# Optimization experiments

Measured on AMD Instinct MI355X. Metric: run time of the kernel, lower is better.

The kernel has to match this reference:

```python
import jax, jax.numpy as jnp
import numpy as np

B, C, N = 2, 128, 784  # batch, channels, spatial tokens (28x28)
TEMPERATURE = 11.313708498984761  # sqrt(C)


def setup_inputs() -> dict:
    key = jax.random.key(0)
    kq, kk, kv = jax.random.split(key, 3)
    q = jax.random.normal(kq, (B, C, N), dtype=jnp.float32)
    k = jax.random.normal(kk, (B, C, N), dtype=jnp.float32)
    v = jax.random.normal(kv, (B, C, N), dtype=jnp.float32)
    return {"q": q, "k": k, "v": v}


def reference(q, k, v):
    # dist_func == 'l1' branch of ScaledDotProductAttention (eval mode, dropout=0)
    qs = q / TEMPERATURE                                   # [B, C, Nq]
    # torch: q.unsqueeze(2).repeat -> [B,C,Nk,Nq]; k.unsqueeze(3).repeat -> [B,C,Nk,Nq]
    # broadcast instead of repeat; mean over channel dim 1
    diff = jnp.abs(qs[:, :, None, :] - k[:, :, :, None])   # [B, C, Nk, Nq]
    attn = jnp.mean(diff, axis=1)                          # [B, Nk, Nq]
    attn = jax.nn.softmax(attn, axis=-1)                   # softmax over Nq (last dim)
    # torch.bmm(v, attn.permute(0,2,1)): out[b,c,k] = sum_q v[b,c,q] * attn[b,k,q]
    out = jnp.einsum("bcq,bkq->bck", v, attn)              # [B, C, Nk]
    return (out, attn)
```

## Files before the change

kernel.cpp:

```cpp
#include <hip/hip_runtime.h>
#include <math.h>

constexpr int kB = 2;
constexpr int kC = 128;
constexpr int kN = 784;
constexpr float kInvT = 1.0f / 11.313708498984761f;
constexpr float kInvC = 1.0f / 128.0f;

constexpr size_t kOutElems  = (size_t)kB * kC * kN;
constexpr size_t kAttnElems = (size_t)kB * kN * kN;

__device__ inline float wave_max(float v) {
#pragma unroll
    for (int o = 32; o > 0; o >>= 1) v = fmaxf(v, __shfl_xor(v, o, 64));
    return v;
}
__device__ inline float wave_sum(float v) {
#pragma unroll
    for (int o = 32; o > 0; o >>= 1) v += __shfl_xor(v, o, 64);
    return v;
}

constexpr int TK = 64;
constexpr int TQ = 64;
constexpr int NKT = (kN + TK - 1) / TK;
constexpr int NQT = (kN + TQ - 1) / TQ;
constexpr int CSP = 2;
constexpr int CH = kC / CSP;
constexpr int DSTR = 68;

template <bool USE_WS>
__global__ __launch_bounds__(256) void dist_kernel(const float* __restrict__ qg,
                                                   const float* __restrict__ kg,
                                                   float* __restrict__ D0,
                                                   float* __restrict__ D1) {
    int bid = blockIdx.x;
    const int qt = bid % NQT; bid /= NQT;
    const int kt = bid % NKT; bid /= NKT;
    const int ch = bid & 1;   bid >>= 1;
    const int b  = bid;
    const int k0 = kt * TK;
    const int q0 = qt * TQ;
    const int t  = threadIdx.x;

    __shared__ float ks[CH][DSTR];
    __shared__ float qs[CH][DSTR];

    const float* kb = kg + ((size_t)b * kC + ch * CH) * kN;
    const float* qb = qg + ((size_t)b * kC + ch * CH) * kN;

#pragma unroll
    for (int i = t; i < CH * 16; i += 256) {
        const int c  = i >> 4;
        const int x4 = (i & 15) << 2;
        *reinterpret_cast<float4*>(&ks[c][x4]) =
            *reinterpret_cast<const float4*>(kb + (size_t)c * kN + min(k0 + x4, kN - 4));
        float4 qv = *reinterpret_cast<const float4*>(qb + (size_t)c * kN + min(q0 + x4, kN - 4));
        qv.x *= kInvT; qv.y *= kInvT; qv.z *= kInvT; qv.w *= kInvT;
        *reinterpret_cast<float4*>(&qs[c][x4]) = qv;
    }
    __syncthreads();

    const int qx = (t & 15) << 2;
    const int kx = (t >> 4) << 2;

    float acc[4][4];
#pragma unroll
    for (int i = 0; i < 4; ++i)
#pragma unroll
        for (int j = 0; j < 4; ++j) acc[i][j] = 0.0f;

#pragma unroll 4
    for (int c = 0; c < CH; ++c) {
        const float4 kv = *reinterpret_cast<const float4*>(&ks[c][kx]);
        const float4 qv = *reinterpret_cast<const float4*>(&qs[c][qx]);
        const float kf[4] = {kv.x, kv.y, kv.z, kv.w};
        const float qf[4] = {qv.x, qv.y, qv.z, qv.w};
#pragma unroll
        for (int i = 0; i < 4; ++i)
#pragma unroll
            for (int j = 0; j < 4; ++j)
                acc[i][j] += fabsf(qf[j] - kf[i]);
    }

    const int qcol = q0 + qx;
    if (qcol < kN) {
        float* dst = (USE_WS && ch) ? D1 : D0;
#pragma unroll
        for (int i = 0; i < 4; ++i) {
            const int krow = k0 + kx + i;
            if (krow < kN) {
                const size_t off = ((size_t)b * kN + krow) * kN + qcol;
                if (USE_WS) {
                    *reinterpret_cast<float4*>(dst + off) =
                        make_float4(acc[i][0], acc[i][1], acc[i][2], acc[i][3]);
                } else {
                    atomicAdd(&D0[off + 0], acc[i][0]);
                    atomicAdd(&D0[off + 1], acc[i][1]);
                    atomicAdd(&D0[off + 2], acc[i][2]);
                    atomicAdd(&D0[off + 3], acc[i][3]);
                }
            }
        }
    }
}

template <bool SUM2>
__global__ __launch_bounds__(256) void softmax_kernel(float* __restrict__ A,
                                                      const float* __restrict__ W) {
    const size_t row = (size_t)blockIdx.x * kN;
    float4* A4 = reinterpret_cast<float4*>(A + row);
    const float4* W4 = reinterpret_cast<const float4*>(W + row);
    const int t = threadIdx.x;
    const int lane = t & 63, wid = t >> 6;
    const bool act = t < (kN / 4);
    __shared__ float xred[4];

    float4 x = make_float4(-1e30f, -1e30f, -1e30f, -1e30f);
    if (act) {
        x = A4[t];
        if (SUM2) {
            const float4 w = W4[t];
            x.x += w.x; x.y += w.y; x.z += w.z; x.w += w.w;
        }
    }

    float m = fmaxf(fmaxf(x.x, x.y), fmaxf(x.z, x.w));
    m = wave_max(m);
    if (lane == 0) xred[wid] = m;
    __syncthreads();
    m = fmaxf(fmaxf(xred[0], xred[1]), fmaxf(xred[2], xred[3]));
    __syncthreads();

    float4 p;
    p.x = __expf((x.x - m) * kInvC);
    p.y = __expf((x.y - m) * kInvC);
    p.z = __expf((x.z - m) * kInvC);
    p.w = __expf((x.w - m) * kInvC);
    float lsum = p.x + p.y + p.z + p.w;
    lsum = wave_sum(lsum);
    if (lane == 0) xred[wid] = lsum;
    __syncthreads();
    const float inv = 1.0f / (xred[0] + xred[1] + xred[2] + xred[3]);
    if (act) {
        p.x *= inv; p.y *= inv; p.z *= inv; p.w *= inv;
        A4[t] = p;
    }
}

constexpr int BKT = 64;
constexpr int NKT2 = (kN + BKT - 1) / BKT;
constexpr int QSP = 14;
constexpr int QPB = kN / QSP;
constexpr int QCH = 28;
constexpr int BSTR = 68;

template <bool ATOMIC>
__global__ __launch_bounds__(256) void bmm_stage1(const float* __restrict__ vg,
                                                  const float* __restrict__ attn,
                                                  float* __restrict__ P) {
    int bid = blockIdx.x;
    const int qs = bid % QSP;   bid /= QSP;
    const int kt = bid % NKT2;  bid /= NKT2;
    const int ct = bid & 1;     bid >>= 1;
    const int b  = bid;
    const int k0 = kt * BKT;
    const int c0 = ct * 64;
    const int qb0 = qs * QPB;
    const int t  = threadIdx.x;

    __shared__ float vT[QCH][BSTR];
    __shared__ float aT[QCH][BSTR];

    const int cc = t >> 2;
    const int j1 = t & 3;
    const int j2 = j1 + 4;
    const int c0l = (t >> 4) << 2;
    const int k0l = (t & 15) << 2;

    float acc[4][4];
#pragma unroll
    for (int i = 0; i < 4; ++i)
#pragma unroll
        for (int j = 0; j < 4; ++j) acc[i][j] = 0.0f;

    const float* vb = vg + ((size_t)b * kC + c0) * kN;
    const float* ab = attn + (size_t)b * kN * kN;
    const int krow_st = min(k0 + cc, kN - 1);

    for (int qc = 0; qc < QPB; qc += QCH) {
        const int q0 = qb0 + qc;
        const float4 vv1 = *reinterpret_cast<const float4*>(vb + (size_t)cc * kN + q0 + 4 * j1);
        const float4 av1 = *reinterpret_cast<const float4*>(ab + (size_t)krow_st * kN + q0 + 4 * j1);
        float4 vv2, av2;
        const bool has2 = (j2 < 7);
        if (has2) {
            vv2 = *reinterpret_cast<const float4*>(vb + (size_t)cc * kN + q0 + 4 * j2);
            av2 = *reinterpret_cast<const float4*>(ab + (size_t)krow_st * kN + q0 + 4 * j2);
        }
        __syncthreads();
        {
            const int r1 = 4 * j1;
            vT[r1 + 0][cc] = vv1.x; vT[r1 + 1][cc] = vv1.y;
            vT[r1 + 2][cc] = vv1.z; vT[r1 + 3][cc] = vv1.w;
            aT[r1 + 0][cc] = av1.x; aT[r1 + 1][cc] = av1.y;
            aT[r1 + 2][cc] = av1.z; aT[r1 + 3][cc] = av1.w;
            if (has2) {
                const int r2 = 4 * j2;
                vT[r2 + 0][cc] = vv2.x; vT[r2 + 1][cc] = vv2.y;
                vT[r2 + 2][cc] = vv2.z; vT[r2 + 3][cc] = vv2.w;
                aT[r2 + 0][cc] = av2.x; aT[r2 + 1][cc] = av2.y;
                aT[r2 + 2][cc] = av2.z; aT[r2 + 3][cc] = av2.w;
            }
        }
        __syncthreads();

#pragma unroll
        for (int qq = 0; qq < QCH; ++qq) {
            const float4 vf4 = *reinterpret_cast<const float4*>(&vT[qq][c0l]);
            const float4 af4 = *reinterpret_cast<const float4*>(&aT[qq][k0l]);
            const float vf[4] = {vf4.x, vf4.y, vf4.z, vf4.w};
            const float af[4] = {af4.x, af4.y, af4.z, af4.w};
#pragma unroll
            for (int i = 0; i < 4; ++i)
#pragma unroll
                for (int j = 0; j < 4; ++j) acc[i][j] += vf[i] * af[j];
        }
    }

    if (ATOMIC) {
#pragma unroll
        for (int i = 0; i < 4; ++i) {
            const int c = c0 + c0l + i;
#pragma unroll
            for (int j = 0; j < 4; ++j) {
                const int krow = k0 + k0l + j;
                if (krow < kN)
                    atomicAdd(&P[((size_t)b * kC + c) * kN + krow], acc[i][j]);
            }
        }
    } else if (k0 + k0l < kN) {
#pragma unroll
        for (int i = 0; i < 4; ++i) {
            const int c = c0 + c0l + i;
            *reinterpret_cast<float4*>(
                P + (((size_t)qs * kB + b) * kC + c) * kN + k0 + k0l) =
                make_float4(acc[i][0], acc[i][1], acc[i][2], acc[i][3]);
        }
    }
}

__global__ __launch_bounds__(256) void reduce_kernel(const float* __restrict__ P,
                                                     float* __restrict__ out) {
    const int idx = blockIdx.x * 256 + threadIdx.x;
    const float4* p = reinterpret_cast<const float4*>(P) + idx;
    float4 s = p[0];
#pragma unroll
    for (int qs = 1; qs < QSP; ++qs) {
        const float4 v = p[(size_t)qs * (kOutElems / 4)];
        s.x += v.x; s.y += v.y; s.z += v.z; s.w += v.w;
    }
    reinterpret_cast<float4*>(out)[idx] = s;
}

extern "C" void kernel_launch(void* const* d_in, const int* in_sizes, int n_in,
                              void* d_out, int out_size, void* d_ws, size_t ws_size,
                              hipStream_t stream) {
    const float* q = (const float*)d_in[0];
    const float* k = (const float*)d_in[1];
    const float* v = (const float*)d_in[2];

    float* out  = (float*)d_out;
    float* attn = out + kOutElems;
    float* P    = (float*)d_ws;
    float* D1   = P + (size_t)QSP * kOutElems;

    const size_t need = ((size_t)QSP * kOutElems + kAttnElems) * sizeof(float);

    if (ws_size >= need) {
        dist_kernel<true><<<kB * CSP * NKT * NQT, 256, 0, stream>>>(q, k, attn, D1);
        softmax_kernel<true><<<kB * kN, 256, 0, stream>>>(attn, D1);
        bmm_stage1<false><<<kB * 2 * NKT2 * QSP, 256, 0, stream>>>(v, attn, P);
        reduce_kernel<<<(int)(kOutElems / 4 / 256), 256, 0, stream>>>(P, out);
    } else {
        hipMemsetAsync(attn, 0, kAttnElems * sizeof(float), stream);
        hipMemsetAsync(out, 0, kOutElems * sizeof(float), stream);
        dist_kernel<false><<<kB * CSP * NKT * NQT, 256, 0, stream>>>(q, k, attn, nullptr);
        softmax_kernel<false><<<kB * kN, 256, 0, stream>>>(attn, attn);
        bmm_stage1<true><<<kB * 2 * NKT2 * QSP, 256, 0, stream>>>(v, attn, out);
    }
}
```

Before: 93.44 us.

## Replace split-K FP32 bmm and reduce with single fp16 MFMA GEMM kernel

The final v·attnᵀ product now runs in one kernel using 16x16x32 fp16 MFMA instructions. It stages v and attn tiles in shared memory as fp16, with register prefetch of the next K chunk. The previous version split the Q dimension 14 ways, wrote partial results to a workspace and summed them in a separate reduce kernel. That pass and its workspace traffic are gone, but the grid drops to 52 blocks, which underfills the GPU, and the inputs lose precision when converted to fp16.

```diff
diff --git a/kernel.cpp b/kernel.cpp
--- a/kernel.cpp
+++ b/kernel.cpp
@@ -148,119 +148,107 @@
     }
 }
 
-constexpr int BKT = 64;
-constexpr int NKT2 = (kN + BKT - 1) / BKT;
-constexpr int QSP = 14;
-constexpr int QPB = kN / QSP;
-constexpr int QCH = 28;
-constexpr int BSTR = 68;
-
-template <bool ATOMIC>
-__global__ __launch_bounds__(256) void bmm_stage1(const float* __restrict__ vg,
-                                                  const float* __restrict__ attn,
-                                                  float* __restrict__ P) {
+typedef _Float16 half4v __attribute__((ext_vector_type(4)));
+typedef _Float16 half8v __attribute__((ext_vector_type(8)));
+typedef float f32x4 __attribute__((ext_vector_type(4)));
+
+constexpr int GM = 64;
+constexpr int GN = 64;
+constexpr int GK = 128;
+constexpr int NCH = (kN + GK - 1) / GK;
+constexpr int NKT3 = (kN + GN - 1) / GN;
+constexpr int LSTR = 136;
+
+__global__ __launch_bounds__(256) void bmm_mfma(const float* __restrict__ vg,
+                                                const float* __restrict__ attn,
+                                                float* __restrict__ out) {
     int bid = blockIdx.x;
-    const int qs = bid % QSP;   bid /= QSP;
-    const int kt = bid % NKT2;  bid /= NKT2;
-    const int ct = bid & 1;     bid >>= 1;
+    const int kt = bid % NKT3; bid /= NKT3;
+    const int ct = bid & 1;    bid >>= 1;
     const int b  = bid;
-    const int k0 = kt * BKT;
-    const int c0 = ct * 64;
-    const int qb0 = qs * QPB;
+    const int k0 = kt * GN;
+    const int c0 = ct * GM;
     const int t  = threadIdx.x;
-
-    __shared__ float vT[QCH][BSTR];
-    __shared__ float aT[QCH][BSTR];
-
-    const int cc = t >> 2;
-    const int j1 = t & 3;
-    const int j2 = j1 + 4;
-    const int c0l = (t >> 4) << 2;
-    const int k0l = (t & 15) << 2;
-
-    float acc[4][4];
-#pragma unroll
-    for (int i = 0; i < 4; ++i)
-#pragma unroll
-        for (int j = 0; j < 4; ++j) acc[i][j] = 0.0f;
+    const int lane = t & 63;
+    const int w = t >> 6;
+
+    __shared__ _Float16 vs[GM][LSTR];
+    __shared__ _Float16 as_[GN][LSTR];
 
     const float* vb = vg + ((size_t)b * kC + c0) * kN;
     const float* ab = attn + (size_t)b * kN * kN;
-    const int krow_st = min(k0 + cc, kN - 1);
-
-    for (int qc = 0; qc < QPB; qc += QCH) {
-        const int q0 = qb0 + qc;
-        const float4 vv1 = *reinterpret_cast<const float4*>(vb + (size_t)cc * kN + q0 + 4 * j1);
-        const float4 av1 = *reinterpret_cast<const float4*>(ab + (size_t)krow_st * kN + q0 + 4 * j1);
-        float4 vv2, av2;
-        const bool has2 = (j2 < 7);
-        if (has2) {
-            vv2 = *reinterpret_cast<const float4*>(vb + (size_t)cc * kN + q0 + 4 * j2);
-            av2 = *reinterpret_cast<const float4*>(ab + (size_t)krow_st * kN + q0 + 4 * j2);
-        }
+
+    const int col4 = t & 31;
+    const int rb   = t >> 5;
+
+    float4 pv[8], pa[8];
+
+    auto load_chunk = [&](int chnk) {
+        const int qv = chnk * GK + 4 * col4;
+        const bool qok = qv < kN;
+#pragma unroll
+        for (int i = 0; i < 8; ++i) {
+            const int row = rb + 8 * i;
+            pv[i] = qok ? *reinterpret_cast<const float4*>(vb + (size_t)row * kN + qv)
+                        : make_float4(0.f, 0.f, 0.f, 0.f);
+            const int krow = k0 + row;
+            pa[i] = (qok && krow < kN)
+                        ? *reinterpret_cast<const float4*>(ab + (size_t)krow * kN + qv)
+                        : make_float4(0.f, 0.f, 0.f, 0.f);
+        }
+    };
+
+    auto store_chunk = [&]() {
+        const int col = 4 * col4;
+#pragma unroll
+        for (int i = 0; i < 8; ++i) {
+            const int row = rb + 8 * i;
+            half4v hv = {(_Float16)pv[i].x, (_Float16)pv[i].y,
+                         (_Float16)pv[i].z, (_Float16)pv[i].w};
+            *reinterpret_cast<half4v*>(&vs[row][col]) = hv;
+            half4v ha = {(_Float16)pa[i].x, (_Float16)pa[i].y,
+                         (_Float16)pa[i].z, (_Float16)pa[i].w};
+            *reinterpret_cast<half4v*>(&as_[row][col]) = ha;
+        }
+    };
+
+    f32x4 acc[4] = {};
+
+    const int arow = 16 * w + (lane & 15);
+    const int brow0 = lane & 15;
+    const int kgrp = (lane >> 4) * 8;
+
+    load_chunk(0);
+    for (int chnk = 0; chnk < NCH; ++chnk) {
         __syncthreads();
-        {
-            const int r1 = 4 * j1;
-            vT[r1 + 0][cc] = vv1.x; vT[r1 + 1][cc] = vv1.y;
-            vT[r1 + 2][cc] = vv1.z; vT[r1 + 3][cc] = vv1.w;
-            aT[r1 + 0][cc] = av1.x; aT[r1 + 1][cc] = av1.y;
-            aT[r1 + 2][cc] = av1.z; aT[r1 + 3][cc] = av1.w;
-            if (has2) {
-                const int r2 = 4 * j2;
-                vT[r2 + 0][cc] = vv2.x; vT[r2 + 1][cc] = vv2.y;
-                vT[r2 + 2][cc] = vv2.z; vT[r2 + 3][cc] = vv2.w;
-                aT[r2 + 0][cc] = av2.x; aT[r2 + 1][cc] = av2.y;
-                aT[r2 + 2][cc] = av2.z; aT[r2 + 3][cc] = av2.w;
+        store_chunk();
+        __syncthreads();
+        if (chnk + 1 < NCH) load_chunk(chnk + 1);
+
+#pragma unroll
+        for (int ks = 0; ks < GK / 32; ++ks) {
+            const int koff = ks * 32 + kgrp;
+            const half8v av = *reinterpret_cast<const half8v*>(&vs[arow][koff]);
+#pragma unroll
+            for (int n = 0; n < 4; ++n) {
+                const half8v bv =
+                    *reinterpret_cast<const half8v*>(&as_[16 * n + brow0][koff]);
+                acc[n] = __builtin_amdgcn_mfma_f32_16x16x32_f16(av, bv, acc[n], 0, 0, 0);
             }
         }
-        __syncthreads();
-
-#pragma unroll
-        for (int qq = 0; qq < QCH; ++qq) {
-            const float4 vf4 = *reinterpret_cast<const float4*>(&vT[qq][c0l]);
-            const float4 af4 = *reinterpret_cast<const float4*>(&aT[qq][k0l]);
-            const float vf[4] = {vf4.x, vf4.y, vf4.z, vf4.w};
-            const float af[4] = {af4.x, af4.y, af4.z, af4.w};
-#pragma unroll
-            for (int i = 0; i < 4; ++i)
-#pragma unroll
-                for (int j = 0; j < 4; ++j) acc[i][j] += vf[i] * af[j];
-        }
-    }
-
-    if (ATOMIC) {
-#pragma unroll
-        for (int i = 0; i < 4; ++i) {
-            const int c = c0 + c0l + i;
-#pragma unroll
-            for (int j = 0; j < 4; ++j) {
-                const int krow = k0 + k0l + j;
-                if (krow < kN)
-                    atomicAdd(&P[((size_t)b * kC + c) * kN + krow], acc[i][j]);
-            }
-        }
-    } else if (k0 + k0l < kN) {
-#pragma unroll
-        for (int i = 0; i < 4; ++i) {
-            const int c = c0 + c0l + i;
-            *reinterpret_cast<float4*>(
-                P + (((size_t)qs * kB + b) * kC + c) * kN + k0 + k0l) =
-                make_float4(acc[i][0], acc[i][1], acc[i][2], acc[i][3]);
-        }
-    }
-}
-
-__global__ __launch_bounds__(256) void reduce_kernel(const float* __restrict__ P,
-                                                     float* __restrict__ out) {
-    const int idx = blockIdx.x * 256 + threadIdx.x;
-    const float4* p = reinterpret_cast<const float4*>(P) + idx;
-    float4 s = p[0];
-#pragma unroll
-    for (int qs = 1; qs < QSP; ++qs) {
-        const float4 v = p[(size_t)qs * (kOutElems / 4)];
-        s.x += v.x; s.y += v.y; s.z += v.z; s.w += v.w;
-    }
-    reinterpret_cast<float4*>(out)[idx] = s;
+    }
+
+    const int crow = c0 + 16 * w + (lane >> 4) * 4;
+    const int kc = k0 + (lane & 15);
+#pragma unroll
+    for (int n = 0; n < 4; ++n) {
+        const int kcol = kc + 16 * n;
+        if (kcol < kN) {
+            float* op = out + ((size_t)b * kC + crow) * kN + kcol;
+#pragma unroll
+            for (int r = 0; r < 4; ++r) op[(size_t)r * kN] = acc[n][r];
+        }
+    }
 }
 
 extern "C" void kernel_launch(void* const* d_in, const int* in_sizes, int n_in,
@@ -272,21 +260,18 @@
 
     float* out  = (float*)d_out;
     float* attn = out + kOutElems;
-    float* P    = (float*)d_ws;
-    float* D1   = P + (size_t)QSP * kOutElems;
-
-    const size_t need = ((size_t)QSP * kOutElems + kAttnElems) * sizeof(float);
+    float* D1   = (float*)d_ws;
+
+    const size_t need = kAttnElems * sizeof(float);
 
     if (ws_size >= need) {
         dist_kernel<true><<<kB * CSP * NKT * NQT, 256, 0, stream>>>(q, k, attn, D1);
         softmax_kernel<true><<<kB * kN, 256, 0, stream>>>(attn, D1);
-        bmm_stage1<false><<<kB * 2 * NKT2 * QSP, 256, 0, stream>>>(v, attn, P);
-        reduce_kernel<<<(int)(kOutElems / 4 / 256), 256, 0, stream>>>(P, out);
+        bmm_mfma<<<kB * 2 * NKT3, 256, 0, stream>>>(v, attn, out);
     } else {
         hipMemsetAsync(attn, 0, kAttnElems * sizeof(float), stream);
-        hipMemsetAsync(out, 0, kOutElems * sizeof(float), stream);
         dist_kernel<false><<<kB * CSP * NKT * NQT, 256, 0, stream>>>(q, k, attn, nullptr);
         softmax_kernel<false><<<kB * kN, 256, 0, stream>>>(attn, attn);
-        bmm_stage1<true><<<kB * 2 * NKT2 * QSP, 256, 0, stream>>>(v, attn, out);
-    }
-}
+        bmm_mfma<<<kB * 2 * NKT3, 256, 0, stream>>>(v, attn, out);
+    }
+}
```

Result: slower. 107.2 us (+14.7%).
